# Performance work log

Measured on AMD Instinct MI355X. Metric: run time of the kernel, lower is better.

## Reference

```python
import jax, jax.numpy as jnp
import numpy as np

N, E, IN, H = 10000, 320000, 128, 64

def setup_inputs() -> dict:
    key = jax.random.key(0)
    ks = jax.random.split(key, 6)
    x = jax.random.normal(ks[0], (N, IN), dtype=jnp.float32)
    edge_index = jax.random.randint(ks[1], (2, E), 0, N)
    edge_weight = jax.random.uniform(ks[2], (E,), dtype=jnp.float32)
    W_rel = jax.random.normal(ks[3], (IN, H), dtype=jnp.float32) / np.float32(np.sqrt(IN))
    W_root = jax.random.normal(ks[4], (IN, H), dtype=jnp.float32) / np.float32(np.sqrt(IN))
    b = jnp.zeros((H,), dtype=jnp.float32)
    return {"x": x, "edge_index": edge_index, "edge_weight": edge_weight,
            "W_rel": W_rel, "W_root": W_root, "b": b}

def reference(x, edge_index, edge_weight, W_rel, W_root, b):
    # GraphConv (PyG): out_i = W_rel @ sum_{j->i} e_ji * x_j + W_root @ x_i + b
    src, dst = edge_index[0], edge_index[1]
    msgs = x[src] * edge_weight[:, None]                    # [E, IN] gather
    agg = jax.ops.segment_sum(msgs, dst, num_segments=N)    # [N, IN] scatter-add
    z = agg @ W_rel + x @ W_root + b                        # [N, H]
    # (activation=None, dropout inactive in eval, no BN)
    adj = jax.nn.sigmoid(z @ z.T)                           # [N, N] inner-product decoder
    return adj, z
```

## Files before the change

kernel.cpp:

```cpp
#include <hip/hip_runtime.h>
#include <hip/hip_bf16.h>
#include <stdint.h>

#define N_NODES 10000
#define N_EDGES 320000
#define DIM_IN  128
#define DIM_H   64
#define SSTR    72
#define CSTR    132

typedef __attribute__((ext_vector_type(8))) short  short8;
typedef __attribute__((ext_vector_type(4))) float  f32x4;

__device__ __forceinline__ unsigned short f2bf(float f) {
    union { float f; unsigned int i; } v; v.f = f;
    unsigned int u = v.i;
    return (unsigned short)((u + 0x7fffu + ((u >> 16) & 1u)) >> 16);
}

__global__ void hist_kernel(const int* __restrict__ ei, int* __restrict__ deg) {
    int e = blockIdx.x * blockDim.x + threadIdx.x;
    if (e < N_EDGES) atomicAdd(&deg[ei[N_EDGES + e]], 1);
}

__global__ void __launch_bounds__(1024) scan_kernel(const int* __restrict__ deg,
                                                    int* __restrict__ offs,
                                                    int* __restrict__ cursor) {
    __shared__ int part[1024];
    int t = threadIdx.x;
    int base = t * 10;
    int local[10];
    int s = 0;
    for (int i = 0; i < 10; ++i) {
        int idx = base + i;
        int d = (idx < N_NODES) ? deg[idx] : 0;
        local[i] = d; s += d;
    }
    part[t] = s;
    __syncthreads();
    for (int o = 1; o < 1024; o <<= 1) {
        int add = (t >= o) ? part[t - o] : 0;
        __syncthreads();
        part[t] += add;
        __syncthreads();
    }
    int run = part[t] - s;
    for (int i = 0; i < 10; ++i) {
        int idx = base + i;
        if (idx < N_NODES) { offs[idx] = run; cursor[idx] = run; run += local[i]; }
    }
    if (t == 1023) offs[N_NODES] = part[1023];
}

__global__ void bucket_kernel(const int* __restrict__ ei, int* __restrict__ cursor,
                              int* __restrict__ esorted) {
    int e = blockIdx.x * blockDim.x + threadIdx.x;
    if (e < N_EDGES) {
        int d = ei[N_EDGES + e];
        int slot = atomicAdd(&cursor[d], 1);
        esorted[slot] = e;
    }
}

__global__ void __launch_bounds__(64) agg_dense_kernel(
    const float* __restrict__ x,
    const int* __restrict__ ei,
    const float* __restrict__ ew,
    const float* __restrict__ wrel,
    const float* __restrict__ wroot,
    const float* __restrict__ bias,
    const int* __restrict__ offs,
    const int* __restrict__ esorted,
    float* __restrict__ out)
{
    int i = blockIdx.x;
    int lane = threadIdx.x;
    __shared__ float aggL[DIM_IN];
    __shared__ float xL[DIM_IN];

    int beg = offs[i], end = offs[i + 1];
    const float2* xrow_i = (const float2*)(x + (size_t)i * DIM_IN);
    float2 xi = xrow_i[lane];
    float a0 = 0.f, a1 = 0.f;
    for (int p = beg; p < end; ++p) {
        int e = esorted[p];
        int s = ei[e];
        float w = ew[e];
        float2 xv = ((const float2*)(x + (size_t)s * DIM_IN))[lane];
        a0 += w * xv.x;
        a1 += w * xv.y;
    }
    aggL[2 * lane]     = a0;
    aggL[2 * lane + 1] = a1;
    xL[2 * lane]       = xi.x;
    xL[2 * lane + 1]   = xi.y;
    __syncthreads();

    int h = lane;
    float acc = bias[h];
    for (int k = 0; k < DIM_IN; ++k) {
        acc += aggL[k] * wrel[k * DIM_H + h];
        acc += xL[k]   * wroot[k * DIM_H + h];
    }
    out[(size_t)N_NODES * N_NODES + (size_t)i * DIM_H + h] = acc;
}

__global__ void __launch_bounds__(256) gemm_sig_kernel(float* __restrict__ out)
{
    const float* zf = out + (size_t)N_NODES * N_NODES;
    __shared__ __align__(16) unsigned short sAB[2 * 128 * SSTR];
    unsigned short* sA = sAB;
    unsigned short* sB = sAB + 128 * SSTR;

    int t    = threadIdx.x;
    int lane = t & 63;
    int wave = t >> 6;
    int wm = wave >> 1, wn = wave & 1;
    int j0 = blockIdx.x * 128;
    int i0 = blockIdx.y * 128;
    int l15  = lane & 15;
    int quad = lane >> 4;

    {
        int r  = t >> 4;
        int c4 = (t & 15) << 2;
        #pragma unroll
        for (int pass = 0; pass < 8; ++pass) {
            int row = pass * 16 + r;
            int ga = i0 + row; if (ga >= N_NODES) ga = N_NODES - 1;
            int gb = j0 + row; if (gb >= N_NODES) gb = N_NODES - 1;
            float4 va = *(const float4*)(zf + (size_t)ga * DIM_H + c4);
            float4 vb = *(const float4*)(zf + (size_t)gb * DIM_H + c4);
            ushort4 ha, hb;
            ha.x = f2bf(va.x); ha.y = f2bf(va.y); ha.z = f2bf(va.z); ha.w = f2bf(va.w);
            hb.x = f2bf(vb.x); hb.y = f2bf(vb.y); hb.z = f2bf(vb.z); hb.w = f2bf(vb.w);
            *(ushort4*)(&sA[row * SSTR + c4]) = ha;
            *(ushort4*)(&sB[row * SSTR + c4]) = hb;
        }
    }
    __syncthreads();

    f32x4 acc[4][4];
    #pragma unroll
    for (int a = 0; a < 4; ++a)
        #pragma unroll
        for (int b = 0; b < 4; ++b) acc[a][b] = (f32x4)0.f;

    #pragma unroll
    for (int s = 0; s < 2; ++s) {
        int kb = quad * 8 + s * 32;
        short8 af[4], bfr[4];
        #pragma unroll
        for (int mi = 0; mi < 4; ++mi)
            af[mi] = *(const short8*)(&sA[(wm * 64 + mi * 16 + l15) * SSTR + kb]);
        #pragma unroll
        for (int ni = 0; ni < 4; ++ni)
            bfr[ni] = *(const short8*)(&sB[(wn * 64 + ni * 16 + l15) * SSTR + kb]);
        #pragma unroll
        for (int mi = 0; mi < 4; ++mi)
            #pragma unroll
            for (int ni = 0; ni < 4; ++ni)
                acc[mi][ni] = __builtin_amdgcn_mfma_f32_16x16x32_bf16(
                    af[mi], bfr[ni], acc[mi][ni], 0, 0, 0);
    }

    float* sC = (float*)sAB;
    #pragma unroll
    for (int half = 0; half < 2; ++half) {
        __syncthreads();
        if (wm == half) {
            #pragma unroll
            for (int mi = 0; mi < 4; ++mi)
                #pragma unroll
                for (int ni = 0; ni < 4; ++ni)
                    #pragma unroll
                    for (int r = 0; r < 4; ++r)
                        sC[(mi * 16 + quad * 4 + r) * CSTR + wn * 64 + ni * 16 + l15]
                            = acc[mi][ni][r];
        }
        __syncthreads();
        int i0h = i0 + half * 64;
        #pragma unroll
        for (int it = 0; it < 8; ++it) {
            int idx = it * 256 + t;
            int row = idx >> 5;
            int c4  = (idx & 31) << 2;
            f32x4 v = *(const f32x4*)&sC[row * CSTR + c4];
            f32x4 sg;
            sg.x = 1.0f / (1.0f + __expf(-v.x));
            sg.y = 1.0f / (1.0f + __expf(-v.y));
            sg.z = 1.0f / (1.0f + __expf(-v.z));
            sg.w = 1.0f / (1.0f + __expf(-v.w));
            int grow = i0h + row;
            int gcol = j0 + c4;
            if (grow < N_NODES && gcol + 3 < N_NODES) {
                __builtin_nontemporal_store(
                    sg, (f32x4*)(out + (size_t)grow * N_NODES + gcol));
            }
        }
    }
}

extern "C" void kernel_launch(void* const* d_in, const int* in_sizes, int n_in,
                              void* d_out, int out_size, void* d_ws, size_t ws_size,
                              hipStream_t stream) {
    const float* x     = (const float*)d_in[0];
    const int*   ei    = (const int*)d_in[1];
    const float* ew    = (const float*)d_in[2];
    const float* wrel  = (const float*)d_in[3];
    const float* wroot = (const float*)d_in[4];
    const float* bias  = (const float*)d_in[5];
    float* out = (float*)d_out;

    char* base = (char*)d_out;
    int* esorted = (int*)(base);
    int* deg     = (int*)(base + 1280000);
    int* offs    = (int*)(base + 1320000);
    int* cursor  = (int*)(base + 1360004);

    hipMemsetAsync(deg, 0, N_NODES * sizeof(int), stream);
    hist_kernel<<<(N_EDGES + 255) / 256, 256, 0, stream>>>(ei, deg);
    scan_kernel<<<1, 1024, 0, stream>>>(deg, offs, cursor);
    bucket_kernel<<<(N_EDGES + 255) / 256, 256, 0, stream>>>(ei, cursor, esorted);
    agg_dense_kernel<<<N_NODES, 64, 0, stream>>>(x, ei, ew, wrel, wroot, bias,
                                                 offs, esorted, out);
    dim3 grid((N_NODES + 127) / 128, (N_NODES + 127) / 128);
    gemm_sig_kernel<<<grid, 256, 0, stream>>>(out);
}
```

Before: 521.2 us.

## Precompute bf16 z in workspace, split edge gather across half-waves

The aggregation kernel now has each half-wave process alternate edges with float4 loads and combines the two halves with a cross-lane shuffle. It also writes a bf16 copy of z to the workspace. The GEMM kernel loads that bf16 copy with 16-byte loads instead of re-reading fp32 z and converting it in every tile. Scratch buffers move from the output buffer to the workspace, so it no longer depends on output memory that is later overwritten.

```diff
diff --git a/kernel.cpp b/kernel.cpp
--- a/kernel.cpp
+++ b/kernel.cpp
@@ -10,6 +10,7 @@
 #define CSTR    132
 
 typedef __attribute__((ext_vector_type(8))) short  short8;
+typedef __attribute__((ext_vector_type(8))) unsigned short ushort8;
 typedef __attribute__((ext_vector_type(4))) float  f32x4;
 
 __device__ __forceinline__ unsigned short f2bf(float f) {
@@ -71,29 +72,36 @@
     const float* __restrict__ bias,
     const int* __restrict__ offs,
     const int* __restrict__ esorted,
-    float* __restrict__ out)
+    float* __restrict__ out,
+    unsigned short* __restrict__ zb)
 {
     int i = blockIdx.x;
     int lane = threadIdx.x;
+    int half = lane >> 5;
+    int l32  = lane & 31;
     __shared__ float aggL[DIM_IN];
     __shared__ float xL[DIM_IN];
 
     int beg = offs[i], end = offs[i + 1];
-    const float2* xrow_i = (const float2*)(x + (size_t)i * DIM_IN);
-    float2 xi = xrow_i[lane];
-    float a0 = 0.f, a1 = 0.f;
-    for (int p = beg; p < end; ++p) {
+    f32x4 a = (f32x4)0.f;
+    for (int p = beg + half; p < end; p += 2) {
         int e = esorted[p];
         int s = ei[e];
         float w = ew[e];
-        float2 xv = ((const float2*)(x + (size_t)s * DIM_IN))[lane];
-        a0 += w * xv.x;
-        a1 += w * xv.y;
-    }
-    aggL[2 * lane]     = a0;
-    aggL[2 * lane + 1] = a1;
-    xL[2 * lane]       = xi.x;
-    xL[2 * lane + 1]   = xi.y;
+        f32x4 xv = *(const f32x4*)(x + (size_t)s * DIM_IN + l32 * 4);
+        a += xv * w;
+    }
+    f32x4 b;
+    b.x = __shfl_xor(a.x, 32);
+    b.y = __shfl_xor(a.y, 32);
+    b.z = __shfl_xor(a.z, 32);
+    b.w = __shfl_xor(a.w, 32);
+    a += b;
+    if (half == 0) *(f32x4*)&aggL[l32 * 4] = a;
+
+    float2 xi = ((const float2*)(x + (size_t)i * DIM_IN))[lane];
+    xL[2 * lane]     = xi.x;
+    xL[2 * lane + 1] = xi.y;
     __syncthreads();
 
     int h = lane;
@@ -103,11 +111,12 @@
         acc += xL[k]   * wroot[k * DIM_H + h];
     }
     out[(size_t)N_NODES * N_NODES + (size_t)i * DIM_H + h] = acc;
-}
-
-__global__ void __launch_bounds__(256) gemm_sig_kernel(float* __restrict__ out)
+    zb[(size_t)i * DIM_H + h] = f2bf(acc);
+}
+
+__global__ void __launch_bounds__(256) gemm_sig_kernel(
+    const unsigned short* __restrict__ zb, float* __restrict__ out)
 {
-    const float* zf = out + (size_t)N_NODES * N_NODES;
     __shared__ __align__(16) unsigned short sAB[2 * 128 * SSTR];
     unsigned short* sA = sAB;
     unsigned short* sB = sAB + 128 * SSTR;
@@ -121,22 +130,17 @@
     int l15  = lane & 15;
     int quad = lane >> 4;
 
-    {
-        int r  = t >> 4;
-        int c4 = (t & 15) << 2;
-        #pragma unroll
-        for (int pass = 0; pass < 8; ++pass) {
-            int row = pass * 16 + r;
-            int ga = i0 + row; if (ga >= N_NODES) ga = N_NODES - 1;
-            int gb = j0 + row; if (gb >= N_NODES) gb = N_NODES - 1;
-            float4 va = *(const float4*)(zf + (size_t)ga * DIM_H + c4);
-            float4 vb = *(const float4*)(zf + (size_t)gb * DIM_H + c4);
-            ushort4 ha, hb;
-            ha.x = f2bf(va.x); ha.y = f2bf(va.y); ha.z = f2bf(va.z); ha.w = f2bf(va.w);
-            hb.x = f2bf(vb.x); hb.y = f2bf(vb.y); hb.z = f2bf(vb.z); hb.w = f2bf(vb.w);
-            *(ushort4*)(&sA[row * SSTR + c4]) = ha;
-            *(ushort4*)(&sB[row * SSTR + c4]) = hb;
-        }
+    #pragma unroll
+    for (int pass = 0; pass < 4; ++pass) {
+        int c   = pass * 256 + t;
+        int row = c >> 3;
+        int c8  = (c & 7) << 3;
+        int ga = i0 + row; if (ga >= N_NODES) ga = N_NODES - 1;
+        int gb = j0 + row; if (gb >= N_NODES) gb = N_NODES - 1;
+        ushort8 va = *(const ushort8*)(zb + (size_t)ga * DIM_H + c8);
+        ushort8 vb = *(const ushort8*)(zb + (size_t)gb * DIM_H + c8);
+        *(ushort8*)(&sA[row * SSTR + c8]) = va;
+        *(ushort8*)(&sB[row * SSTR + c8]) = vb;
     }
     __syncthreads();
 
@@ -212,18 +216,19 @@
     const float* bias  = (const float*)d_in[5];
     float* out = (float*)d_out;
 
-    char* base = (char*)d_out;
-    int* esorted = (int*)(base);
-    int* deg     = (int*)(base + 1280000);
-    int* offs    = (int*)(base + 1320000);
-    int* cursor  = (int*)(base + 1360004);
+    char* base = (char*)d_ws;
+    unsigned short* zb = (unsigned short*)(base);
+    int* esorted = (int*)(base + 1280000);
+    int* deg     = (int*)(base + 2560000);
+    int* offs    = (int*)(base + 2600000);
+    int* cursor  = (int*)(base + 2640004);
 
     hipMemsetAsync(deg, 0, N_NODES * sizeof(int), stream);
     hist_kernel<<<(N_EDGES + 255) / 256, 256, 0, stream>>>(ei, deg);
     scan_kernel<<<1, 1024, 0, stream>>>(deg, offs, cursor);
     bucket_kernel<<<(N_EDGES + 255) / 256, 256, 0, stream>>>(ei, cursor, esorted);
     agg_dense_kernel<<<N_NODES, 64, 0, stream>>>(x, ei, ew, wrel, wroot, bias,
-                                                 offs, esorted, out);
+                                                 offs, esorted, out, zb);
     dim3 grid((N_NODES + 127) / 128, (N_NODES + 127) / 128);
-    gemm_sig_kernel<<<grid, 256, 0, stream>>>(out);
-}
+    gemm_sig_kernel<<<grid, 256, 0, stream>>>(zb, out);
+}
```

Result: no change. 517.4 us (-0.7%).
